# Performance work log

Hardware: AMD Instinct MI355X
Metric: run time of the kernel (lower is better)

## Reference

```python
import jax, jax.numpy as jnp
import numpy as np

DT = 1.0
EPS = 1e-6


def setup_inputs() -> dict:
    key = jax.random.key(0)
    k1, k2, k3, k4 = jax.random.split(key, 4)
    batch, in_ch, out_ch, state_dim, T = 16, 256, 256, 256, 8192
    u = jax.random.normal(k1, (batch, in_ch, T), dtype=jnp.float32)
    raw_lambda = jax.random.normal(k2, (state_dim,), dtype=jnp.float32)
    B_c = jax.random.normal(k3, (in_ch, state_dim), dtype=jnp.float32) * (1.0 / in_ch ** 0.5)
    C = jax.random.normal(k4, (state_dim, out_ch), dtype=jnp.float32) * (1.0 / state_dim ** 0.5)
    return {"u": u, "raw_lambda": raw_lambda, "B_c": B_c, "C": C}


def reference(u, raw_lambda, B_c, C):
    # ZOH discretization of diagonal SSM (all-real here since raw_lambda is real)
    lam = -jax.nn.softplus(raw_lambda)                 # (N,)
    A_d = jnp.exp(lam * DT)                            # (N,)
    factor = jnp.where(jnp.abs(lam) > EPS, (A_d - 1.0) / lam, jnp.full_like(lam, DT))
    B_d = B_c * factor[None, :]                        # (in_ch, N)

    # Precompute driving inputs for every step in one big GEMM: (T, B, N)
    x = jnp.einsum('bct,cn->tbn', u, B_d)

    batch, state_dim = u.shape[0], raw_lambda.shape[0]

    def step(s, x_t):
        s = s * A_d[None, :] + x_t                     # diagonal recurrence
        return s, s

    s0 = jnp.zeros((batch, state_dim), dtype=u.dtype)
    _, states = jax.lax.scan(step, s0, x)              # states: (T, B, N)

    # Project all states at once: y (B, out_ch, T)
    y = jnp.einsum('tbn,no->bot', states, C)
    return y
```

## Files before the change

### kernel.cpp

```cpp
#include <hip/hip_runtime.h>
#include <math.h>

typedef __attribute__((ext_vector_type(8)))  short short8;
typedef __attribute__((ext_vector_type(16))) float f32x16;

#define B_  16
#define C_  256
#define N_  256
#define O_  256
#define T_  8192
#define L_  64
#define NC_ 128

#define GLL16(gptr, lptr) \
  __builtin_amdgcn_global_load_lds((const __attribute__((address_space(1))) void*)(gptr), \
                                   (__attribute__((address_space(3))) void*)(lptr), 16, 0, 0)

__device__ inline unsigned short f2bf(float x) {
    unsigned u = __float_as_uint(x);
    u += 0x7fff + ((u >> 16) & 1);
    return (unsigned short)(u >> 16);
}
__device__ inline float bf2f(unsigned short h) {
    return __uint_as_float(((unsigned)h) << 16);
}
__device__ inline unsigned cvtpk(float a, float b) {
    unsigned r;
    asm("v_cvt_pk_bf16_f32 %0, %1, %2" : "=v"(r) : "v"(a), "v"(b));
    return r;
}
__device__ inline f32x16 zero16() {
    f32x16 z;
    #pragma unroll
    for (int i = 0; i < 16; ++i) z[i] = 0.f;
    return z;
}

__global__ __launch_bounds__(256) void k_prep(
    const float* __restrict__ raw_lambda, const float* __restrict__ B_c,
    const float* __restrict__ Cmat,
    float* __restrict__ Ad, float* __restrict__ AL,
    unsigned short* __restrict__ BdKf, unsigned short* __restrict__ CKf)
{
    const int r = blockIdx.x;
    const int t = threadIdx.x;
    const int kk = r >> 5, ri = r & 31;
    const int s = ri >> 4, hi = (ri >> 3) & 1, j = ri & 7;
    const int nt = t >> 5, l = (hi << 5) | (t & 31);
    const int idx = (((kk * 8 + nt) * 2 + s) * 64 + l) * 8 + j;

    if (blockIdx.y == 0) {
        const float x  = raw_lambda[t];
        const float sp = (x > 20.f) ? x : log1pf(expf(x));
        const float lam = -sp;
        const float ad  = expf(lam);
        const float factor = (fabsf(lam) > 1e-6f) ? (ad - 1.f) / lam : 1.f;
        if (r == 0) {
            Ad[t] = ad;
            float al = ad;
            #pragma unroll
            for (int i = 0; i < 6; ++i) al *= al;
            AL[t] = al;
        }
        BdKf[idx] = f2bf(B_c[r * N_ + t] * factor);
    } else {
        CKf[idx] = f2bf(Cmat[r * O_ + t]);
    }
}

#define LDFRAG(MAT, kk, buf) { \
    _Pragma("unroll") \
    for (int q_ = 0; q_ < 2; ++q_) \
        _Pragma("unroll") \
        for (int s_ = 0; s_ < 2; ++s_) \
            fb[buf][q_ * 2 + s_] = *(const short8*)( \
                (MAT) + ((((kk) * 8 + 2 * w + q_) * 2 + s_) * 64 + l) * 8); }

__global__ __launch_bounds__(256, 2) void k_phaseA(
    const float* __restrict__ u, const unsigned short* __restrict__ BdKf,
    const float* __restrict__ Ad, float* __restrict__ p_last,
    unsigned short* __restrict__ X, int doX)
{
    __shared__ __align__(16) unsigned short ut[16896];

    const int k = blockIdx.x, b = blockIdx.y;
    const int tid = threadIdx.x;
    const int w = tid >> 6, l = tid & 63, lo = l & 31, hi = l >> 5;
    const float* ub = u + (size_t)b * C_ * T_ + k * L_;

    const float adq0 = Ad[(2 * w + 0) * 32 + lo];
    const float adq1 = Ad[(2 * w + 1) * 32 + lo];

    float4 v[16];
    #pragma unroll
    for (int q = 0; q < 16; ++q) {
        const int i = q * 256 + tid, cl = i >> 4, t4 = i & 15;
        v[q] = *(const float4*)(ub + (size_t)cl * T_ + t4 * 4);
    }
    {
        unsigned* ud = (unsigned*)ut;
        #pragma unroll
        for (int q = 0; q < 16; ++q) {
            const int i = q * 256 + tid, cl = i >> 4, t4 = i & 15;
            float4 a = v[q], p;
            p.x = __shfl_xor(a.x, 16); p.y = __shfl_xor(a.y, 16);
            p.z = __shfl_xor(a.z, 16); p.w = __shfl_xor(a.w, 16);
            const bool odd = (cl & 1) != 0;
            const float l0 = odd ? p.z : a.x, h0 = odd ? a.z : p.x;
            const float l1 = odd ? p.w : a.y, h1 = odd ? a.w : p.y;
            const int r0 = odd ? 2 : 0;
            const int nb = cl >> 3, jd = (cl >> 1) & 3;
            const int tA = 4 * t4 + r0, tB = tA + 1;
            const int xsw = (tA >> 3) & 3;
            ud[tA * 132 + (((nb ^ xsw) << 2) | jd)] = cvtpk(l0, h0);
            ud[tB * 132 + (((nb ^ xsw) << 2) | jd)] = cvtpk(l1, h1);
        }
    }
    __syncthreads();

    f32x16 a00 = zero16(), a01 = zero16(), a10 = zero16(), a11 = zero16();
    short8 fb[3][4];
    LDFRAG(BdKf, 0, 0)
    LDFRAG(BdKf, 1, 1)
    #pragma unroll
    for (int kk = 0; kk < 8; ++kk) {
        if (kk < 6) LDFRAG(BdKf, kk + 2, (kk + 2) % 3)
        #pragma unroll
        for (int s = 0; s < 2; ++s) {
            const int blk8 = kk * 4 + s * 2 + hi;
            const int tA2 = lo, tB2 = 32 + lo;
            const short8 fa0 = *(const short8*)(ut + tA2 * 264 + ((blk8 ^ ((tA2 >> 3) & 3)) << 3));
            const short8 fa1 = *(const short8*)(ut + tB2 * 264 + ((blk8 ^ ((tB2 >> 3) & 3)) << 3));
            const short8 fb0 = fb[kk % 3][0 * 2 + s];
            const short8 fb1 = fb[kk % 3][1 * 2 + s];
            a00 = __builtin_amdgcn_mfma_f32_32x32x16_bf16(fa0, fb0, a00, 0, 0, 0);
            a01 = __builtin_amdgcn_mfma_f32_32x32x16_bf16(fa0, fb1, a01, 0, 0, 0);
            a10 = __builtin_amdgcn_mfma_f32_32x32x16_bf16(fa1, fb0, a10, 0, 0, 0);
            a11 = __builtin_amdgcn_mfma_f32_32x32x16_bf16(fa1, fb1, a11, 0, 0, 0);
        }
    }

    if (doX) {
        unsigned* Xd = (unsigned*)X + (size_t)(k * B_ + b) * 8192;
        #pragma unroll
        for (int f = 0; f < 4; ++f) {
            const f32x16 a = (f == 0) ? a00 : (f == 1) ? a01 : (f == 2) ? a10 : a11;
            unsigned dw[8];
            #pragma unroll
            for (int d = 0; d < 8; ++d)
                dw[d] = cvtpk(a[2 * d], a[2 * d + 1]);
            unsigned* base = Xd + w * 2048 + f * 512 + l * 4;
            *(int4*)(base)       = *(const int4*)&dw[0];
            *(int4*)(base + 256) = *(const int4*)&dw[4];
        }
    }

    {
        float p[2];
        #pragma unroll
        for (int q = 0; q < 2; ++q) {
            const float ad = q ? adq1 : adq0;
            const float ad2 = ad * ad, ad4 = ad2 * ad2, ad8 = ad4 * ad4;
            const float ad16 = ad8 * ad8, ad32 = ad16 * ad16;
            float full[2];
            #pragma unroll
            for (int tt = 0; tt < 2; ++tt) {
                const f32x16 a = (tt == 0) ? (q == 0 ? a00 : a01)
                                           : (q == 0 ? a10 : a11);
                float v2[4];
                #pragma unroll
                for (int g = 0; g < 4; ++g)
                    v2[g] = fmaf(fmaf(fmaf(a[4*g], ad, a[4*g+1]), ad, a[4*g+2]), ad, a[4*g+3]);
                const float H = fmaf(fmaf(fmaf(v2[0], ad8, v2[1]), ad8, v2[2]), ad8, v2[3]);
                float P = hi ? H : H * ad4;
                P += __shfl_xor(P, 32);
                full[tt] = P;
            }
            p[q] = fmaf(full[0], ad32, full[1]);
        }
        if (hi == 0) {
            float* dst = p_last + (size_t)(k * B_ + b) * N_;
            dst[(2 * w + 0) * 32 + lo] = p[0];
            dst[(2 * w + 1) * 32 + lo] = p[1];
        }
    }
}

__global__ __launch_bounds__(256) void k_phaseB(
    const float* __restrict__ p_last, const float* __restrict__ AL,
    float* __restrict__ carry)
{
    __shared__ float buf[32 * 256];
    const int b = blockIdx.x, n = threadIdx.x;
    const float al = AL[n];
    float cur = 0.f;
    for (int kc = 0; kc < 4; ++kc) {
        __syncthreads();
        #pragma unroll
        for (int q = 0; q < 32; ++q)
            buf[q * 256 + n] = p_last[((size_t)(kc * 32 + q) * B_ + b) * N_ + n];
        __syncthreads();
        #pragma unroll
        for (int q = 0; q < 32; ++q) {
            carry[((size_t)(kc * 32 + q) * B_ + b) * N_ + n] = cur;
            cur = fmaf(cur, al, buf[q * 256 + n]);
        }
    }
}

__global__ __launch_bounds__(256, 2) void k_phaseC(
    const unsigned short* __restrict__ X, const unsigned short* __restrict__ CKf,
    const float* __restrict__ Ad, const float* __restrict__ carry,
    float* __restrict__ y)
{
    __shared__ __align__(16) unsigned short xs[16896];

    const int k = blockIdx.x, b = blockIdx.y;
    const int tid = threadIdx.x;
    const int w = tid >> 6, l = tid & 63, lo = l & 31, hi = l >> 5;
    const int t0 = k * L_;

    {
        const char* src = (const char*)X + (size_t)(k * B_ + b) * 32768;
        #pragma unroll
        for (int q = 0; q < 8; ++q)
            GLL16(src + q * 4096 + w * 1024 + (l << 4),
                  (char*)xs + q * 4096 + w * 1024);
    }
    const float cv = carry[(size_t)(k * B_ + b) * N_ + tid];
    const float ad = Ad[tid];
    __syncthreads();

    unsigned arr[2][2][8];
    {
        const unsigned* xd = (const unsigned*)xs;
        const int w2 = tid >> 6, q2 = (tid >> 5) & 1, lo2 = tid & 31;
        #pragma unroll
        for (int tt = 0; tt < 2; ++tt)
            #pragma unroll
            for (int h2 = 0; h2 < 2; ++h2) {
                const unsigned* p = xd + w2 * 2048 + (tt * 2 + q2) * 512
                                       + (h2 * 32 + lo2) * 4;
                *(int4*)&arr[tt][h2][0] = *(const int4*)(p);
                *(int4*)&arr[tt][h2][4] = *(const int4*)(p + 256);
            }
    }
    __syncthreads();

    {
        const int nb = tid >> 3, nl = tid & 7;
        float s = cv;
        #pragma unroll
        for (int tt = 0; tt < 2; ++tt)
            #pragma unroll
            for (int g = 0; g < 4; ++g)
                #pragma unroll
                for (int h2 = 0; h2 < 2; ++h2) {
                    const unsigned d0 = arr[tt][h2][2 * g];
                    const unsigned d1 = arr[tt][h2][2 * g + 1];
                    const int tb = tt * 32 + 8 * g + 4 * h2;
                    const int swz = (((nb ^ ((tb >> 3) & 3)) << 3) | nl);
                    s = fmaf(s, ad, bf2f((unsigned short)(d0 & 0xffff)));
                    xs[(tb + 0) * 264 + swz] = f2bf(s);
                    s = fmaf(s, ad, bf2f((unsigned short)(d0 >> 16)));
                    xs[(tb + 1) * 264 + swz] = f2bf(s);
                    s = fmaf(s, ad, bf2f((unsigned short)(d1 & 0xffff)));
                    xs[(tb + 2) * 264 + swz] = f2bf(s);
                    s = fmaf(s, ad, bf2f((unsigned short)(d1 >> 16)));
                    xs[(tb + 3) * 264 + swz] = f2bf(s);
                }
    }
    __syncthreads();

    f32x16 c00 = zero16(), c01 = zero16(), c10 = zero16(), c11 = zero16();
    short8 fb[3][4];
    LDFRAG(CKf, 0, 0)
    LDFRAG(CKf, 1, 1)
    #pragma unroll
    for (int kk = 0; kk < 8; ++kk) {
        if (kk < 6) LDFRAG(CKf, kk + 2, (kk + 2) % 3)
        #pragma unroll
        for (int s = 0; s < 2; ++s) {
            short8 fa[2];
            #pragma unroll
            for (int tt = 0; tt < 2; ++tt) {
                const int t = tt * 32 + lo;
                const int blk = (kk * 4 + s * 2 + hi) ^ ((t >> 3) & 3);
                fa[tt] = *(const short8*)(xs + t * 264 + blk * 8);
            }
            const short8 fb0 = fb[kk % 3][0 * 2 + s];
            const short8 fb1 = fb[kk % 3][1 * 2 + s];
            c00 = __builtin_amdgcn_mfma_f32_32x32x16_bf16(fa[0], fb0, c00, 0, 0, 0);
            c01 = __builtin_amdgcn_mfma_f32_32x32x16_bf16(fa[0], fb1, c01, 0, 0, 0);
            c10 = __builtin_amdgcn_mfma_f32_32x32x16_bf16(fa[1], fb0, c10, 0, 0, 0);
            c11 = __builtin_amdgcn_mfma_f32_32x32x16_bf16(fa[1], fb1, c11, 0, 0, 0);
        }
    }

    #pragma unroll
    for (int tt = 0; tt < 2; ++tt)
        #pragma unroll
        for (int q = 0; q < 2; ++q) {
            const f32x16 a = (tt == 0) ? (q == 0 ? c00 : c01) : (q == 0 ? c10 : c11);
            const int o = (2 * w + q) * 32 + lo;
            float* yo = y + ((size_t)b * O_ + o) * T_ + t0 + tt * 32 + hi * 4;
            #pragma unroll
            for (int g = 0; g < 4; ++g) {
                float4 vv;
                vv.x = a[g * 4 + 0]; vv.y = a[g * 4 + 1];
                vv.z = a[g * 4 + 2]; vv.w = a[g * 4 + 3];
                *(float4*)(yo + g * 8) = vv;
            }
        }
}

__device__ __forceinline__ void gemm1_rc(
    const float* __restrict__ u, const unsigned short* __restrict__ BdKf,
    int b, int k, unsigned short* xs, unsigned short* ut, unsigned short* bb)
{
    const int tid = threadIdx.x;
    const int w = tid >> 6, l = tid & 63, lo = l & 31, hi = l >> 5;
    const int t0 = k * L_;
    f32x16 a00 = zero16(), a01 = zero16(), a10 = zero16(), a11 = zero16();
    for (int kk = 0; kk < 8; ++kk) {
        #pragma unroll
        for (int q = 0; q < 2; ++q) {
            const int i = q * 256 + tid, cl = i >> 4, t4 = i & 15;
            const float4 v = *(const float4*)(
                u + ((size_t)b * C_ + kk * 32 + cl) * T_ + t0 + t4 * 4);
            ut[(t4 * 4 + 0) * 40 + cl] = f2bf(v.x);
            ut[(t4 * 4 + 1) * 40 + cl] = f2bf(v.y);
            ut[(t4 * 4 + 2) * 40 + cl] = f2bf(v.z);
            ut[(t4 * 4 + 3) * 40 + cl] = f2bf(v.w);
        }
        {
            const unsigned short* src = BdKf + kk * 8192;
            #pragma unroll
            for (int q = 0; q < 4; ++q) {
                const int i16 = q * 256 + tid;
                *(int4*)(bb + i16 * 8) = *(const int4*)(src + i16 * 8);
            }
        }
        __syncthreads();
        #pragma unroll
        for (int s = 0; s < 2; ++s) {
            const short8 fa0 = *(const short8*)(ut + (0 * 32 + lo) * 40 + s * 16 + hi * 8);
            const short8 fa1 = *(const short8*)(ut + (1 * 32 + lo) * 40 + s * 16 + hi * 8);
            const short8 fb0 = *(const short8*)(bb + (((2 * w + 0) * 2 + s) * 64 + l) * 8);
            const short8 fb1 = *(const short8*)(bb + (((2 * w + 1) * 2 + s) * 64 + l) * 8);
            a00 = __builtin_amdgcn_mfma_f32_32x32x16_bf16(fa0, fb0, a00, 0, 0, 0);
            a01 = __builtin_amdgcn_mfma_f32_32x32x16_bf16(fa0, fb1, a01, 0, 0, 0);
            a10 = __builtin_amdgcn_mfma_f32_32x32x16_bf16(fa1, fb0, a10, 0, 0, 0);
            a11 = __builtin_amdgcn_mfma_f32_32x32x16_bf16(fa1, fb1, a11, 0, 0, 0);
        }
        __syncthreads();
    }
    #pragma unroll
    for (int tt = 0; tt < 2; ++tt)
        #pragma unroll
        for (int q = 0; q < 2; ++q) {
            const f32x16 a = (tt == 0) ? (q == 0 ? a00 : a01) : (q == 0 ? a10 : a11);
            const int n = (2 * w + q) * 32 + lo;
            #pragma unroll
            for (int g = 0; g < 4; ++g)
                #pragma unroll
                for (int p = 0; p < 2; ++p)
                    *(unsigned*)(xs + n * 66 + tt * 32 + hi * 4 + g * 8 + p * 2)
                        = f2bf(a[g * 4 + 2 * p]) | ((unsigned)f2bf(a[g * 4 + 2 * p + 1]) << 16);
        }
    __syncthreads();
}

__global__ __launch_bounds__(256) void k_phaseC_rc(
    const float* __restrict__ u, const unsigned short* __restrict__ BdKf,
    const unsigned short* __restrict__ CKf, const float* __restrict__ Ad,
    const float* __restrict__ carry, float* __restrict__ y)
{
    __shared__ __align__(16) unsigned short xs[16896];
    __shared__ __align__(16) unsigned short ut[2560];
    __shared__ __align__(16) unsigned short bb[8192];

    const int k = blockIdx.x, b = blockIdx.y;
    const int tid = threadIdx.x;
    const int w = tid >> 6, l = tid & 63, lo = l & 31, hi = l >> 5;
    const int t0 = k * L_;

    gemm1_rc(u, BdKf, b, k, xs, ut, bb);

    {
        const float a = Ad[tid];
        float s = carry[((size_t)k * B_ + b) * N_ + tid];
        float st[64];
        #pragma unroll
        for (int m = 0; m < 32; ++m) {
            const unsigned dw = *(const unsigned*)(xs + tid * 66 + 2 * m);
            s = fmaf(s, a, bf2f((unsigned short)(dw & 0xffff)));  st[2 * m] = s;
            s = fmaf(s, a, bf2f((unsigned short)(dw >> 16)));     st[2 * m + 1] = s;
        }
        __syncthreads();
        #pragma unroll
        for (int t = 0; t < 64; ++t) xs[t * 264 + tid] = f2bf(st[t]);
    }
    __syncthreads();

    f32x16 c00 = zero16(), c01 = zero16(), c10 = zero16(), c11 = zero16();
    for (int kk = 0; kk < 8; ++kk) {
        __syncthreads();
        {
            const unsigned short* src = CKf + kk * 8192;
            #pragma unroll
            for (int q = 0; q < 4; ++q) {
                const int i16 = q * 256 + tid;
                *(int4*)(bb + i16 * 8) = *(const int4*)(src + i16 * 8);
            }
        }
        __syncthreads();
        #pragma unroll
        for (int s = 0; s < 2; ++s) {
            const short8 fa0 = *(const short8*)(xs + (0 * 32 + lo) * 264 + kk * 32 + s * 16 + hi * 8);
            const short8 fa1 = *(const short8*)(xs + (1 * 32 + lo) * 264 + kk * 32 + s * 16 + hi * 8);
            const short8 fb0 = *(const short8*)(bb + (((2 * w + 0) * 2 + s) * 64 + l) * 8);
            const short8 fb1 = *(const short8*)(bb + (((2 * w + 1) * 2 + s) * 64 + l) * 8);
            c00 = __builtin_amdgcn_mfma_f32_32x32x16_bf16(fa0, fb0, c00, 0, 0, 0);
            c01 = __builtin_amdgcn_mfma_f32_32x32x16_bf16(fa0, fb1, c01, 0, 0, 0);
            c10 = __builtin_amdgcn_mfma_f32_32x32x16_bf16(fa1, fb0, c10, 0, 0, 0);
            c11 = __builtin_amdgcn_mfma_f32_32x32x16_bf16(fa1, fb1, c11, 0, 0, 0);
        }
    }

    #pragma unroll
    for (int tt = 0; tt < 2; ++tt)
        #pragma unroll
        for (int q = 0; q < 2; ++q) {
            const f32x16 a = (tt == 0) ? (q == 0 ? c00 : c01) : (q == 0 ? c10 : c11);
            const int o = (2 * w + q) * 32 + lo;
            float* yo = y + ((size_t)b * O_ + o) * T_ + t0 + tt * 32 + hi * 4;
            #pragma unroll
            for (int g = 0; g < 4; ++g) {
                float4 vv;
                vv.x = a[g * 4 + 0]; vv.y = a[g * 4 + 1];
                vv.z = a[g * 4 + 2]; vv.w = a[g * 4 + 3];
                *(float4*)(yo + g * 8) = vv;
            }
        }
}

extern "C" void kernel_launch(void* const* d_in, const int* in_sizes, int n_in,
                              void* d_out, int out_size, void* d_ws, size_t ws_size,
                              hipStream_t stream)
{
    const float* u  = (const float*)d_in[0];
    const float* rl = (const float*)d_in[1];
    const float* Bc = (const float*)d_in[2];
    const float* Cm = (const float*)d_in[3];
    float* y  = (float*)d_out;
    char*  ws = (char*)d_ws;

    float* Ad     = (float*)(ws + 0);
    float* AL     = (float*)(ws + 1024);
    float* p_last = (float*)(ws + 2048);
    float* carry  = (float*)(ws + 2048 + 2097152);
    unsigned short* BdKf = (unsigned short*)(ws + 2048 + 2 * 2097152);
    unsigned short* CKf  = (unsigned short*)(ws + 2048 + 2 * 2097152 + 131072);
    unsigned short* X    = (unsigned short*)(ws + 2048 + 2 * 2097152 + 2 * 131072);
    const size_t need = 2048 + 2ull * 2097152 + 2ull * 131072
                      + (size_t)NC_ * B_ * 32768;
    const int doX = (ws_size >= need) ? 1 : 0;

    k_prep  <<<dim3(256, 2),  dim3(256), 0, stream>>>(rl, Bc, Cm, Ad, AL, BdKf, CKf);
    k_phaseA<<<dim3(NC_, B_), dim3(256), 0, stream>>>(u, BdKf, Ad, p_last, X, doX);
    k_phaseB<<<dim3(B_),      dim3(256), 0, stream>>>(p_last, AL, carry);
    if (doX)
        k_phaseC<<<dim3(NC_, B_), dim3(256), 0, stream>>>(X, CKf, Ad, carry, y);
    else
        k_phaseC_rc<<<dim3(NC_, B_), dim3(256), 0, stream>>>(u, BdKf, CKf, Ad, carry, y);
}
```

Measured before the change: 107.5 us.

## Fuse chunked scan phases into one kernel with decoupled-lookback carry

```diff
diff --git a/kernel.cpp b/kernel.cpp
--- a/kernel.cpp
+++ b/kernel.cpp
@@ -11,10 +11,6 @@
 #define T_  8192
 #define L_  64
 #define NC_ 128
-
-#define GLL16(gptr, lptr) \
-  __builtin_amdgcn_global_load_lds((const __attribute__((address_space(1))) void*)(gptr), \
-                                   (__attribute__((address_space(3))) void*)(lptr), 16, 0, 0)
 
 __device__ inline unsigned short f2bf(float x) {
     unsigned u = __float_as_uint(x);
@@ -76,29 +72,37 @@
             fb[buf][q_ * 2 + s_] = *(const short8*)( \
                 (MAT) + ((((kk) * 8 + 2 * w + q_) * 2 + s_) * 64 + l) * 8); }
 
-__global__ __launch_bounds__(256, 2) void k_phaseA(
-    const float* __restrict__ u, const unsigned short* __restrict__ BdKf,
-    const float* __restrict__ Ad, float* __restrict__ p_last,
-    unsigned short* __restrict__ X, int doX)
+__global__ __launch_bounds__(256, 2) void k_fused(
+    const float* __restrict__ u,
+    const unsigned short* __restrict__ BdKf, const unsigned short* __restrict__ CKf,
+    const float* __restrict__ Ad, const float* __restrict__ AL,
+    unsigned* __restrict__ flags, unsigned* __restrict__ partU,
+    int* __restrict__ ticket, float* __restrict__ y)
 {
-    __shared__ __align__(16) unsigned short ut[16896];
-
-    const int k = blockIdx.x, b = blockIdx.y;
+    __shared__ __align__(16) unsigned short xs[16896];
+    __shared__ int vid_s;
+
     const int tid = threadIdx.x;
     const int w = tid >> 6, l = tid & 63, lo = l & 31, hi = l >> 5;
-    const float* ub = u + (size_t)b * C_ * T_ + k * L_;
+
+    if (tid == 0) vid_s = atomicAdd(ticket, 1);
+    __syncthreads();
+    const int vid = vid_s;
+    const int b = vid & 15, k = vid >> 4;
+    const int t0 = k * L_;
+    const float* ub = u + (size_t)b * C_ * T_ + t0;
 
     const float adq0 = Ad[(2 * w + 0) * 32 + lo];
     const float adq1 = Ad[(2 * w + 1) * 32 + lo];
 
-    float4 v[16];
-    #pragma unroll
-    for (int q = 0; q < 16; ++q) {
-        const int i = q * 256 + tid, cl = i >> 4, t4 = i & 15;
-        v[q] = *(const float4*)(ub + (size_t)cl * T_ + t4 * 4);
-    }
-    {
-        unsigned* ud = (unsigned*)ut;
+    {
+        float4 v[16];
+        #pragma unroll
+        for (int q = 0; q < 16; ++q) {
+            const int i = q * 256 + tid, cl = i >> 4, t4 = i & 15;
+            v[q] = *(const float4*)(ub + (size_t)cl * T_ + t4 * 4);
+        }
+        unsigned* ud = (unsigned*)xs;
         #pragma unroll
         for (int q = 0; q < 16; ++q) {
             const int i = q * 256 + tid, cl = i >> 4, t4 = i & 15;
@@ -119,39 +123,26 @@
     __syncthreads();
 
     f32x16 a00 = zero16(), a01 = zero16(), a10 = zero16(), a11 = zero16();
-    short8 fb[3][4];
-    LDFRAG(BdKf, 0, 0)
-    LDFRAG(BdKf, 1, 1)
-    #pragma unroll
-    for (int kk = 0; kk < 8; ++kk) {
-        if (kk < 6) LDFRAG(BdKf, kk + 2, (kk + 2) % 3)
-        #pragma unroll
-        for (int s = 0; s < 2; ++s) {
-            const int blk8 = kk * 4 + s * 2 + hi;
-            const int tA2 = lo, tB2 = 32 + lo;
-            const short8 fa0 = *(const short8*)(ut + tA2 * 264 + ((blk8 ^ ((tA2 >> 3) & 3)) << 3));
-            const short8 fa1 = *(const short8*)(ut + tB2 * 264 + ((blk8 ^ ((tB2 >> 3) & 3)) << 3));
-            const short8 fb0 = fb[kk % 3][0 * 2 + s];
-            const short8 fb1 = fb[kk % 3][1 * 2 + s];
-            a00 = __builtin_amdgcn_mfma_f32_32x32x16_bf16(fa0, fb0, a00, 0, 0, 0);
-            a01 = __builtin_amdgcn_mfma_f32_32x32x16_bf16(fa0, fb1, a01, 0, 0, 0);
-            a10 = __builtin_amdgcn_mfma_f32_32x32x16_bf16(fa1, fb0, a10, 0, 0, 0);
-            a11 = __builtin_amdgcn_mfma_f32_32x32x16_bf16(fa1, fb1, a11, 0, 0, 0);
-        }
-    }
-
-    if (doX) {
-        unsigned* Xd = (unsigned*)X + (size_t)(k * B_ + b) * 8192;
-        #pragma unroll
-        for (int f = 0; f < 4; ++f) {
-            const f32x16 a = (f == 0) ? a00 : (f == 1) ? a01 : (f == 2) ? a10 : a11;
-            unsigned dw[8];
-            #pragma unroll
-            for (int d = 0; d < 8; ++d)
-                dw[d] = cvtpk(a[2 * d], a[2 * d + 1]);
-            unsigned* base = Xd + w * 2048 + f * 512 + l * 4;
-            *(int4*)(base)       = *(const int4*)&dw[0];
-            *(int4*)(base + 256) = *(const int4*)&dw[4];
+    {
+        short8 fb[3][4];
+        LDFRAG(BdKf, 0, 0)
+        LDFRAG(BdKf, 1, 1)
+        #pragma unroll
+        for (int kk = 0; kk < 8; ++kk) {
+            if (kk < 6) LDFRAG(BdKf, kk + 2, (kk + 2) % 3)
+            #pragma unroll
+            for (int s = 0; s < 2; ++s) {
+                const int blk8 = kk * 4 + s * 2 + hi;
+                const int tA2 = lo, tB2 = 32 + lo;
+                const short8 fa0 = *(const short8*)(xs + tA2 * 264 + ((blk8 ^ ((tA2 >> 3) & 3)) << 3));
+                const short8 fa1 = *(const short8*)(xs + tB2 * 264 + ((blk8 ^ ((tB2 >> 3) & 3)) << 3));
+                const short8 fb0 = fb[kk % 3][0 * 2 + s];
+                const short8 fb1 = fb[kk % 3][1 * 2 + s];
+                a00 = __builtin_amdgcn_mfma_f32_32x32x16_bf16(fa0, fb0, a00, 0, 0, 0);
+                a01 = __builtin_amdgcn_mfma_f32_32x32x16_bf16(fa0, fb1, a01, 0, 0, 0);
+                a10 = __builtin_amdgcn_mfma_f32_32x32x16_bf16(fa1, fb0, a10, 0, 0, 0);
+                a11 = __builtin_amdgcn_mfma_f32_32x32x16_bf16(fa1, fb1, a11, 0, 0, 0);
+            }
         }
     }
 
@@ -179,56 +170,32 @@
             p[q] = fmaf(full[0], ad32, full[1]);
         }
         if (hi == 0) {
-            float* dst = p_last + (size_t)(k * B_ + b) * N_;
-            dst[(2 * w + 0) * 32 + lo] = p[0];
-            dst[(2 * w + 1) * 32 + lo] = p[1];
-        }
-    }
-}
-
-__global__ __launch_bounds__(256) void k_phaseB(
-    const float* __restrict__ p_last, const float* __restrict__ AL,
-    float* __restrict__ carry)
-{
-    __shared__ float buf[32 * 256];
-    const int b = blockIdx.x, n = threadIdx.x;
-    const float al = AL[n];
-    float cur = 0.f;
-    for (int kc = 0; kc < 4; ++kc) {
-        __syncthreads();
-        #pragma unroll
-        for (int q = 0; q < 32; ++q)
-            buf[q * 256 + n] = p_last[((size_t)(kc * 32 + q) * B_ + b) * N_ + n];
-        __syncthreads();
-        #pragma unroll
-        for (int q = 0; q < 32; ++q) {
-            carry[((size_t)(kc * 32 + q) * B_ + b) * N_ + n] = cur;
-            cur = fmaf(cur, al, buf[q * 256 + n]);
-        }
-    }
-}
-
-__global__ __launch_bounds__(256, 2) void k_phaseC(
-    const unsigned short* __restrict__ X, const unsigned short* __restrict__ CKf,
-    const float* __restrict__ Ad, const float* __restrict__ carry,
-    float* __restrict__ y)
-{
-    __shared__ __align__(16) unsigned short xs[16896];
-
-    const int k = blockIdx.x, b = blockIdx.y;
-    const int tid = threadIdx.x;
-    const int w = tid >> 6, l = tid & 63, lo = l & 31, hi = l >> 5;
-    const int t0 = k * L_;
-
-    {
-        const char* src = (const char*)X + (size_t)(k * B_ + b) * 32768;
-        #pragma unroll
-        for (int q = 0; q < 8; ++q)
-            GLL16(src + q * 4096 + w * 1024 + (l << 4),
-                  (char*)xs + q * 4096 + w * 1024);
-    }
-    const float cv = carry[(size_t)(k * B_ + b) * N_ + tid];
-    const float ad = Ad[tid];
+            unsigned* dst = partU + (size_t)(b * 128 + k) * 256;
+            __hip_atomic_store(dst + (2 * w + 0) * 32 + lo, __float_as_uint(p[0]),
+                               __ATOMIC_RELAXED, __HIP_MEMORY_SCOPE_AGENT);
+            __hip_atomic_store(dst + (2 * w + 1) * 32 + lo, __float_as_uint(p[1]),
+                               __ATOMIC_RELAXED, __HIP_MEMORY_SCOPE_AGENT);
+        }
+    }
+    __syncthreads();
+    if (tid == 0)
+        __hip_atomic_store(flags + b * 128 + k, 1u,
+                           __ATOMIC_RELEASE, __HIP_MEMORY_SCOPE_AGENT);
+
+    {
+        unsigned* Xd = (unsigned*)xs;
+        #pragma unroll
+        for (int f = 0; f < 4; ++f) {
+            const f32x16 a = (f == 0) ? a00 : (f == 1) ? a01 : (f == 2) ? a10 : a11;
+            unsigned dw[8];
+            #pragma unroll
+            for (int d = 0; d < 8; ++d)
+                dw[d] = cvtpk(a[2 * d], a[2 * d + 1]);
+            unsigned* base = Xd + w * 2048 + f * 512 + l * 4;
+            *(int4*)(base)       = *(const int4*)&dw[0];
+            *(int4*)(base + 256) = *(const int4*)&dw[4];
+        }
+    }
     __syncthreads();
 
     unsigned arr[2][2][8];
@@ -245,11 +212,30 @@
                 *(int4*)&arr[tt][h2][4] = *(const int4*)(p + 256);
             }
     }
-    __syncthreads();
-
-    {
+
+    float cur = 0.f;
+    {
+        if (tid < k) {
+            const unsigned* fl = flags + b * 128 + tid;
+            while (__hip_atomic_load(fl, __ATOMIC_RELAXED, __HIP_MEMORY_SCOPE_AGENT) == 0u)
+                __builtin_amdgcn_s_sleep(1);
+        }
+        __syncthreads();
+        const float al = AL[tid];
+        const unsigned* pU = partU + (size_t)b * 128 * 256 + tid;
+        #pragma unroll 16
+        for (int j = 0; j < k; ++j) {
+            const float pv = __uint_as_float(
+                __hip_atomic_load(pU + (size_t)j * 256,
+                                  __ATOMIC_RELAXED, __HIP_MEMORY_SCOPE_AGENT));
+            cur = fmaf(cur, al, pv);
+        }
+    }
+
+    {
+        const float ad = Ad[tid];
         const int nb = tid >> 3, nl = tid & 7;
-        float s = cv;
+        float s = cur;
         #pragma unroll
         for (int tt = 0; tt < 2; ++tt)
             #pragma unroll
@@ -273,158 +259,29 @@
     __syncthreads();
 
     f32x16 c00 = zero16(), c01 = zero16(), c10 = zero16(), c11 = zero16();
-    short8 fb[3][4];
-    LDFRAG(CKf, 0, 0)
-    LDFRAG(CKf, 1, 1)
-    #pragma unroll
-    for (int kk = 0; kk < 8; ++kk) {
-        if (kk < 6) LDFRAG(CKf, kk + 2, (kk + 2) % 3)
-        #pragma unroll
-        for (int s = 0; s < 2; ++s) {
-            short8 fa[2];
-            #pragma unroll
-            for (int tt = 0; tt < 2; ++tt) {
-                const int t = tt * 32 + lo;
-                const int blk = (kk * 4 + s * 2 + hi) ^ ((t >> 3) & 3);
-                fa[tt] = *(const short8*)(xs + t * 264 + blk * 8);
-            }
-            const short8 fb0 = fb[kk % 3][0 * 2 + s];
-            const short8 fb1 = fb[kk % 3][1 * 2 + s];
-            c00 = __builtin_amdgcn_mfma_f32_32x32x16_bf16(fa[0], fb0, c00, 0, 0, 0);
-            c01 = __builtin_amdgcn_mfma_f32_32x32x16_bf16(fa[0], fb1, c01, 0, 0, 0);
-            c10 = __builtin_amdgcn_mfma_f32_32x32x16_bf16(fa[1], fb0, c10, 0, 0, 0);
-            c11 = __builtin_amdgcn_mfma_f32_32x32x16_bf16(fa[1], fb1, c11, 0, 0, 0);
-        }
-    }
-
-    #pragma unroll
-    for (int tt = 0; tt < 2; ++tt)
-        #pragma unroll
-        for (int q = 0; q < 2; ++q) {
-            const f32x16 a = (tt == 0) ? (q == 0 ? c00 : c01) : (q == 0 ? c10 : c11);
-            const int o = (2 * w + q) * 32 + lo;
-            float* yo = y + ((size_t)b * O_ + o) * T_ + t0 + tt * 32 + hi * 4;
-            #pragma unroll
-            for (int g = 0; g < 4; ++g) {
-                float4 vv;
-                vv.x = a[g * 4 + 0]; vv.y = a[g * 4 + 1];
-                vv.z = a[g * 4 + 2]; vv.w = a[g * 4 + 3];
-                *(float4*)(yo + g * 8) = vv;
-            }
-        }
-}
-
-__device__ __forceinline__ void gemm1_rc(
-    const float* __restrict__ u, const unsigned short* __restrict__ BdKf,
-    int b, int k, unsigned short* xs, unsigned short* ut, unsigned short* bb)
-{
-    const int tid = threadIdx.x;
-    const int w = tid >> 6, l = tid & 63, lo = l & 31, hi = l >> 5;
-    const int t0 = k * L_;
-    f32x16 a00 = zero16(), a01 = zero16(), a10 = zero16(), a11 = zero16();
-    for (int kk = 0; kk < 8; ++kk) {
-        #pragma unroll
-        for (int q = 0; q < 2; ++q) {
-            const int i = q * 256 + tid, cl = i >> 4, t4 = i & 15;
-            const float4 v = *(const float4*)(
-                u + ((size_t)b * C_ + kk * 32 + cl) * T_ + t0 + t4 * 4);
-            ut[(t4 * 4 + 0) * 40 + cl] = f2bf(v.x);
-            ut[(t4 * 4 + 1) * 40 + cl] = f2bf(v.y);
-            ut[(t4 * 4 + 2) * 40 + cl] = f2bf(v.z);
-            ut[(t4 * 4 + 3) * 40 + cl] = f2bf(v.w);
-        }
-        {
-            const unsigned short* src = BdKf + kk * 8192;
-            #pragma unroll
-            for (int q = 0; q < 4; ++q) {
-                const int i16 = q * 256 + tid;
-                *(int4*)(bb + i16 * 8) = *(const int4*)(src + i16 * 8);
-            }
-        }
-        __syncthreads();
-        #pragma unroll
-        for (int s = 0; s < 2; ++s) {
-            const short8 fa0 = *(const short8*)(ut + (0 * 32 + lo) * 40 + s * 16 + hi * 8);
-            const short8 fa1 = *(const short8*)(ut + (1 * 32 + lo) * 40 + s * 16 + hi * 8);
-            const short8 fb0 = *(const short8*)(bb + (((2 * w + 0) * 2 + s) * 64 + l) * 8);
-            const short8 fb1 = *(const short8*)(bb + (((2 * w + 1) * 2 + s) * 64 + l) * 8);
-            a00 = __builtin_amdgcn_mfma_f32_32x32x16_bf16(fa0, fb0, a00, 0, 0, 0);
-            a01 = __builtin_amdgcn_mfma_f32_32x32x16_bf16(fa0, fb1, a01, 0, 0, 0);
-            a10 = __builtin_amdgcn_mfma_f32_32x32x16_bf16(fa1, fb0, a10, 0, 0, 0);
-            a11 = __builtin_amdgcn_mfma_f32_32x32x16_bf16(fa1, fb1, a11, 0, 0, 0);
-        }
-        __syncthreads();
-    }
-    #pragma unroll
-    for (int tt = 0; tt < 2; ++tt)
-        #pragma unroll
-        for (int q = 0; q < 2; ++q) {
-            const f32x16 a = (tt == 0) ? (q == 0 ? a00 : a01) : (q == 0 ? a10 : a11);
-            const int n = (2 * w + q) * 32 + lo;
-            #pragma unroll
-            for (int g = 0; g < 4; ++g)
+    {
+        short8 fb[3][4];
+        LDFRAG(CKf, 0, 0)
+        LDFRAG(CKf, 1, 1)
+        #pragma unroll
+        for (int kk = 0; kk < 8; ++kk) {
+            if (kk < 6) LDFRAG(CKf, kk + 2, (kk + 2) % 3)
+            #pragma unroll
+            for (int s = 0; s < 2; ++s) {
+                short8 fa[2];
                 #pragma unroll
-                for (int p = 0; p < 2; ++p)
-                    *(unsigned*)(xs + n * 66 + tt * 32 + hi * 4 + g * 8 + p * 2)
-                        = f2bf(a[g * 4 + 2 * p]) | ((unsigned)f2bf(a[g * 4 + 2 * p + 1]) << 16);
-        }
-    __syncthreads();
-}
-
-__global__ __launch_bounds__(256) void k_phaseC_rc(
-    const float* __restrict__ u, const unsigned short* __restrict__ BdKf,
-    const unsigned short* __restrict__ CKf, const float* __restrict__ Ad,
-    const float* __restrict__ carry, float* __restrict__ y)
-{
-    __shared__ __align__(16) unsigned short xs[16896];
-    __shared__ __align__(16) unsigned short ut[2560];
-    __shared__ __align__(16) unsigned short bb[8192];
-
-    const int k = blockIdx.x, b = blockIdx.y;
-    const int tid = threadIdx.x;
-    const int w = tid >> 6, l = tid & 63, lo = l & 31, hi = l >> 5;
-    const int t0 = k * L_;
-
-    gemm1_rc(u, BdKf, b, k, xs, ut, bb);
-
-    {
-        const float a = Ad[tid];
-        float s = carry[((size_t)k * B_ + b) * N_ + tid];
-        float st[64];
-        #pragma unroll
-        for (int m = 0; m < 32; ++m) {
-            const unsigned dw = *(const unsigned*)(xs + tid * 66 + 2 * m);
-            s = fmaf(s, a, bf2f((unsigned short)(dw & 0xffff)));  st[2 * m] = s;
-            s = fmaf(s, a, bf2f((unsigned short)(dw >> 16)));     st[2 * m + 1] = s;
-        }
-        __syncthreads();
-        #pragma unroll
-        for (int t = 0; t < 64; ++t) xs[t * 264 + tid] = f2bf(st[t]);
-    }
-    __syncthreads();
-
-    f32x16 c00 = zero16(), c01 = zero16(), c10 = zero16(), c11 = zero16();
-    for (int kk = 0; kk < 8; ++kk) {
-        __syncthreads();
-        {
-            const unsigned short* src = CKf + kk * 8192;
-            #pragma unroll
-            for (int q = 0; q < 4; ++q) {
-                const int i16 = q * 256 + tid;
-                *(int4*)(bb + i16 * 8) = *(const int4*)(src + i16 * 8);
-            }
-        }
-        __syncthreads();
-        #pragma unroll
-        for (int s = 0; s < 2; ++s) {
-            const short8 fa0 = *(const short8*)(xs + (0 * 32 + lo) * 264 + kk * 32 + s * 16 + hi * 8);
-            const short8 fa1 = *(const short8*)(xs + (1 * 32 + lo) * 264 + kk * 32 + s * 16 + hi * 8);
-            const short8 fb0 = *(const short8*)(bb + (((2 * w + 0) * 2 + s) * 64 + l) * 8);
-            const short8 fb1 = *(const short8*)(bb + (((2 * w + 1) * 2 + s) * 64 + l) * 8);
-            c00 = __builtin_amdgcn_mfma_f32_32x32x16_bf16(fa0, fb0, c00, 0, 0, 0);
-            c01 = __builtin_amdgcn_mfma_f32_32x32x16_bf16(fa0, fb1, c01, 0, 0, 0);
-            c10 = __builtin_amdgcn_mfma_f32_32x32x16_bf16(fa1, fb0, c10, 0, 0, 0);
-            c11 = __builtin_amdgcn_mfma_f32_32x32x16_bf16(fa1, fb1, c11, 0, 0, 0);
+                for (int tt = 0; tt < 2; ++tt) {
+                    const int t = tt * 32 + lo;
+                    const int blk = (kk * 4 + s * 2 + hi) ^ ((t >> 3) & 3);
+                    fa[tt] = *(const short8*)(xs + t * 264 + blk * 8);
+                }
+                const short8 fb0 = fb[kk % 3][0 * 2 + s];
+                const short8 fb1 = fb[kk % 3][1 * 2 + s];
+                c00 = __builtin_amdgcn_mfma_f32_32x32x16_bf16(fa[0], fb0, c00, 0, 0, 0);
+                c01 = __builtin_amdgcn_mfma_f32_32x32x16_bf16(fa[0], fb1, c01, 0, 0, 0);
+                c10 = __builtin_amdgcn_mfma_f32_32x32x16_bf16(fa[1], fb0, c10, 0, 0, 0);
+                c11 = __builtin_amdgcn_mfma_f32_32x32x16_bf16(fa[1], fb1, c11, 0, 0, 0);
+            }
         }
     }
 
@@ -456,22 +313,16 @@
     float* y  = (float*)d_out;
     char*  ws = (char*)d_ws;
 
-    float* Ad     = (float*)(ws + 0);
-    float* AL     = (float*)(ws + 1024);
-    float* p_last = (float*)(ws + 2048);
-    float* carry  = (float*)(ws + 2048 + 2097152);
-    unsigned short* BdKf = (unsigned short*)(ws + 2048 + 2 * 2097152);
-    unsigned short* CKf  = (unsigned short*)(ws + 2048 + 2 * 2097152 + 131072);
-    unsigned short* X    = (unsigned short*)(ws + 2048 + 2 * 2097152 + 2 * 131072);
-    const size_t need = 2048 + 2ull * 2097152 + 2ull * 131072
-                      + (size_t)NC_ * B_ * 32768;
-    const int doX = (ws_size >= need) ? 1 : 0;
-
-    k_prep  <<<dim3(256, 2),  dim3(256), 0, stream>>>(rl, Bc, Cm, Ad, AL, BdKf, CKf);
-    k_phaseA<<<dim3(NC_, B_), dim3(256), 0, stream>>>(u, BdKf, Ad, p_last, X, doX);
-    k_phaseB<<<dim3(B_),      dim3(256), 0, stream>>>(p_last, AL, carry);
-    if (doX)
-        k_phaseC<<<dim3(NC_, B_), dim3(256), 0, stream>>>(X, CKf, Ad, carry, y);
-    else
-        k_phaseC_rc<<<dim3(NC_, B_), dim3(256), 0, stream>>>(u, BdKf, CKf, Ad, carry, y);
-}
+    int*      ticket = (int*)(ws + 0);
+    unsigned* flags  = (unsigned*)(ws + 128);
+    float*    Ad     = (float*)(ws + 8448);
+    float*    AL     = (float*)(ws + 9472);
+    unsigned* partU  = (unsigned*)(ws + 10496);
+    unsigned short* BdKf = (unsigned short*)(ws + 2107648);
+    unsigned short* CKf  = (unsigned short*)(ws + 2238720);
+
+    hipMemsetAsync(d_ws, 0, 8448, stream);
+    k_prep <<<dim3(256, 2),   dim3(256), 0, stream>>>(rl, Bc, Cm, Ad, AL, BdKf, CKf);
+    k_fused<<<dim3(NC_ * B_), dim3(256), 0, stream>>>(u, BdKf, CKf, Ad, AL,
+                                                      flags, partU, ticket, y);
+}
```

Measured after the change: 153.4 us. +42.8%, slower.
